# Kernel tuning notes

Hardware: AMD Instinct MI355X
Metric: run time of the kernel (lower is better)

The kernel has to match this reference:

```python
import jax, jax.numpy as jnp
import numpy as np

B, S, D, H = 2, 2048, 1024, 16
DEPTH = D // H


def setup_inputs() -> dict:
    key = jax.random.key(0)
    ks = jax.random.split(key, 10)
    batch = jax.random.normal(ks[0], (B, S, D), dtype=jnp.float32)
    # variable-length valid rows, like padded batches in the original repo
    lengths = jax.random.randint(ks[1], (B,), S // 2, S + 1)
    mask = jnp.arange(S)[None, :] < lengths[:, None]  # (B, S) bool
    scale = 1.0 / np.sqrt(D)
    Wq = jax.random.normal(ks[2], (D, D), dtype=jnp.float32) * scale
    bq = jnp.zeros((D,), dtype=jnp.float32)
    Wk = jax.random.normal(ks[3], (D, D), dtype=jnp.float32) * scale
    bk = jnp.zeros((D,), dtype=jnp.float32)
    Wv = jax.random.normal(ks[4], (D, D), dtype=jnp.float32) * scale
    bv = jnp.zeros((D,), dtype=jnp.float32)
    Wo = jax.random.normal(ks[5], (D, D), dtype=jnp.float32) * scale
    bo = jnp.zeros((D,), dtype=jnp.float32)
    return {"batch": batch, "mask": mask, "Wq": Wq, "bq": bq, "Wk": Wk,
            "bk": bk, "Wv": Wv, "bv": bv, "Wo": Wo, "bo": bo}


def _split_heads(x):
    # (B, S, D) -> (B, H, S, depth)
    b, s, _ = x.shape
    return x.reshape(b, s, H, DEPTH).transpose(0, 2, 1, 3)


def reference(batch, mask, Wq, bq, Wk, bk, Wv, bv, Wo, bo):
    b, s, _ = batch.shape
    Q = _split_heads(batch @ Wq + bq)
    K = _split_heads(batch @ Wk + bk)
    V = _split_heads(batch @ Wv + bv)
    # scaled dot-product attention with key-padding mask
    logits = jnp.einsum('bhqd,bhkd->bhqk', Q, K) / jnp.sqrt(
        jnp.asarray(DEPTH, dtype=batch.dtype))
    neg = (~mask).astype(batch.dtype) * -1e9  # (B, S)
    logits = logits + neg[:, None, None, :]
    attn = jax.nn.softmax(logits, axis=-1)
    X = jnp.einsum('bhqk,bhkd->bhqd', attn, V)
    X = X.transpose(0, 2, 1, 3).reshape(b, s, D)
    return X @ Wo + bo
```

## Files before the change

kernel.cpp:

```cpp
#include <hip/hip_runtime.h>
#include <hip/hip_bf16.h>

#define DEV __device__ __forceinline__

typedef short bf16x8 __attribute__((ext_vector_type(8)));
typedef float f32x4  __attribute__((ext_vector_type(4)));
typedef float f32x16 __attribute__((ext_vector_type(16)));

#define Bc 2
#define Sc 2048
#define Dc 1024
#define Hc 16

#define OFF_XB    0u
#define OFF_WQKVT 8388608u
#define OFF_WOT   14680064u
#define OFF_Q     16777216u
#define OFF_K     25165824u
#define OFF_VT    33554432u
#define OFF_XA    41943040u
#define OFF_BIASC 50331648u
#define OFF_LENS  50343936u

DEV short f2bf(float f) {
    __hip_bfloat16 h = __float2bfloat16(f);
    union { __hip_bfloat16 h; short s; } u; u.h = h; return u.s;
}

DEV int cvtpk(float lo, float hi_) {
    int r;
    asm("v_cvt_pk_bf16_f32 %0, %1, %2" : "=v"(r) : "v"(lo), "v"(hi_));
    return r;
}

DEV float vexp2(float x) {
    float r;
    asm("v_exp_f32 %0, %1" : "=v"(r) : "v"(x));
    return r;
}

DEV void gload16(const void* g, void* l) {
    __builtin_amdgcn_global_load_lds((const __attribute__((address_space(1))) void*)g,
                                     (__attribute__((address_space(3))) void*)l, 16, 0, 0);
}

union I4BF { int i[4]; bf16x8 v; };

DEV bf16x8 vread(const char* Vc, int row, int grp, int hi16, int rsw) {
    return *(const bf16x8*)(Vc + row * 128 + ((grp + hi16) ^ rsw));
}

__global__ __launch_bounds__(256) void prep_all_kernel(
    const float* __restrict__ batch,
    const float* __restrict__ Wq, const float* __restrict__ Wk,
    const float* __restrict__ Wv, const float* __restrict__ Wo,
    const float* __restrict__ bq, const float* __restrict__ bk, const float* __restrict__ bv,
    const unsigned char* __restrict__ mask,
    short* __restrict__ XB, short* __restrict__ WQKVT, short* __restrict__ WOT,
    float* __restrict__ biasc, int* __restrict__ lens)
{
    __shared__ float tsm[32][33];
    __shared__ int cnt;
    int blk = blockIdx.x, t = threadIdx.x;

    if (blk < 4096) {
        int i = blk * 256 + t;
        float4 v = ((const float4*)batch)[i];
        short4 o;
        o.x = f2bf(v.x); o.y = f2bf(v.y); o.z = f2bf(v.z); o.w = f2bf(v.w);
        ((short4*)XB)[i] = o;
        return;
    }
    if (blk < 8192) {
        int w = blk - 4096, z = w >> 10, tile = w & 1023;
        const float* src; short* dst;
        if (z == 0)      { src = Wq; dst = WQKVT; }
        else if (z == 1) { src = Wk; dst = WQKVT + 1024 * 1024; }
        else if (z == 2) { src = Wv; dst = WQKVT + 2 * 1024 * 1024; }
        else             { src = Wo; dst = WOT; }
        int tx = t & 31, ty = t >> 5;
        int r0 = (tile >> 5) * 32, c0 = (tile & 31) * 32;
#pragma unroll
        for (int i = 0; i < 4; i++)
            tsm[ty + i * 8][tx] = src[(size_t)(r0 + ty + i * 8) * Dc + c0 + tx];
        __syncthreads();
#pragma unroll
        for (int i = 0; i < 4; i++)
            dst[(size_t)(c0 + ty + i * 8) * Dc + r0 + tx] = f2bf(tsm[tx][ty + i * 8]);
        return;
    }
    if (blk == 8192) {
        for (int i = t; i < Dc; i += 256) {
            biasc[i] = bq[i]; biasc[Dc + i] = bk[i]; biasc[2 * Dc + i] = bv[i];
        }
        return;
    }
    {
        int b = blk - 8193;
        bool is_i32 = (mask[1] == 0);
        if (t == 0) cnt = 0;
        __syncthreads();
        int local = 0;
        for (int s = t; s < Sc; s += 256) {
            bool v = is_i32 ? (((const int*)mask)[b * Sc + s] != 0) : (mask[b * Sc + s] != 0);
            local += v ? 1 : 0;
        }
        atomicAdd(&cnt, local);
        __syncthreads();
        if (t == 0) lens[b] = cnt;
    }
}

__global__ __launch_bounds__(256) void vtrans_kernel(const short* __restrict__ V,
                                                     short* __restrict__ VT) {
    __shared__ short t[64][65];
    int tid = threadIdx.x;
    int bh = blockIdx.y, s0 = blockIdx.x * 64;
    int rr = tid >> 2, c4 = (tid & 3) * 16;
    const short* vrow = V + ((size_t)bh * Sc + s0 + rr) * 64 + c4;
    *(bf16x8*)&t[rr][c4]     = *(const bf16x8*)(vrow);
    *(bf16x8*)&t[rr][c4 + 8] = *(const bf16x8*)(vrow + 8);
    __syncthreads();
    bf16x8 a, b2;
#pragma unroll
    for (int i = 0; i < 4; i++) {
        a[i]      = t[c4 + i][rr];
        a[4 + i]  = t[c4 + 8 + i][rr];
        b2[i]     = t[c4 + 4 + i][rr];
        b2[4 + i] = t[c4 + 12 + i][rr];
    }
    short* orow = VT + ((size_t)bh * 64 + rr) * Sc + s0 + c4;
    *(bf16x8*)(orow)     = a;
    *(bf16x8*)(orow + 8) = b2;
}

__global__ __launch_bounds__(256) void gemm_qkv_kernel(
    const short* __restrict__ A, const short* __restrict__ BT, const float* __restrict__ bias,
    short* __restrict__ Qp, short* __restrict__ Kp, short* __restrict__ Vp)
{
    __shared__ short As[128 * 32];
    __shared__ short Bs[128 * 32];
    int tid = threadIdx.x, lane = tid & 63, wave = tid >> 6;
    int l15 = lane & 15, lhi = lane >> 4;
    int bm = blockIdx.x, bn = blockIdx.y;
    int wm = wave >> 1, wn = wave & 1;

    const f32x4 fzero = {0.f, 0.f, 0.f, 0.f};
    f32x4 acc[4][4];
#pragma unroll
    for (int i = 0; i < 4; i++)
#pragma unroll
        for (int j = 0; j < 4; j++) acc[i][j] = fzero;

    const char* Ab = (const char*)A;
    const char* Bb = (const char*)BT;

    for (int k0 = 0; k0 < 1024; k0 += 32) {
#pragma unroll
        for (int i = 0; i < 2; i++) {
            int o = wave * 2048 + i * 1024 + lane * 16;
            int row = o >> 6, cb = o & 63;
            gload16(Ab + ((size_t)(bm * 128 + row) * 1024 + k0) * 2 + cb,
                    (char*)As + wave * 2048 + i * 1024);
            gload16(Bb + ((size_t)(bn * 128 + row) * 1024 + k0) * 2 + cb,
                    (char*)Bs + wave * 2048 + i * 1024);
        }
        __syncthreads();
        bf16x8 af[4], bfv[4];
#pragma unroll
        for (int i = 0; i < 4; i++) {
            af[i]  = *(const bf16x8*)(As + (wm * 64 + i * 16 + l15) * 32 + lhi * 8);
            bfv[i] = *(const bf16x8*)(Bs + (wn * 64 + i * 16 + l15) * 32 + lhi * 8);
        }
#pragma unroll
        for (int i = 0; i < 4; i++)
#pragma unroll
            for (int j = 0; j < 4; j++)
                acc[i][j] = __builtin_amdgcn_mfma_f32_16x16x32_bf16(af[i], bfv[j], acc[i][j], 0, 0, 0);
        __syncthreads();
    }

#pragma unroll
    for (int i = 0; i < 4; i++)
#pragma unroll
        for (int j = 0; j < 4; j++) {
            int c = bn * 128 + wn * 64 + j * 16 + l15;
            float bc = bias[c];
            int rb = bm * 128 + wm * 64 + i * 16 + 4 * lhi;
#pragma unroll
            for (int reg = 0; reg < 4; reg++) {
                int r = rb + reg;
                float v = acc[i][j][reg] + bc;
                int which = c >> 10, cc = c & 1023, h = cc >> 6, d = cc & 63;
                int b = r >> 11, s = r & 2047;
                int bh = b * Hc + h;
                if (which == 0) v *= 0.18033688f;
                short sv = f2bf(v);
                size_t idx = ((size_t)bh * Sc + s) * 64 + d;
                if (which == 0)      Qp[idx] = sv;
                else if (which == 1) Kp[idx] = sv;
                else                 Vp[idx] = sv;
            }
        }
}

__global__ __launch_bounds__(256) void gemm_out_kernel(
    const short* __restrict__ A, const short* __restrict__ BT, const float* __restrict__ bias,
    float* __restrict__ outF)
{
    __shared__ short As[128 * 32];
    __shared__ short Bs[64 * 32];
    int tid = threadIdx.x, lane = tid & 63, wave = tid >> 6;
    int l15 = lane & 15, lhi = lane >> 4;
    int bm = blockIdx.x, bn = blockIdx.y;

    const f32x4 fzero = {0.f, 0.f, 0.f, 0.f};
    f32x4 acc[2][4];
#pragma unroll
    for (int i = 0; i < 2; i++)
#pragma unroll
        for (int j = 0; j < 4; j++) acc[i][j] = fzero;

    const char* Ab = (const char*)A;
    const char* Bb = (const char*)BT;

    for (int k0 = 0; k0 < 1024; k0 += 32) {
#pragma unroll
        for (int i = 0; i < 2; i++) {
            int o = wave * 2048 + i * 1024 + lane * 16;
            int row = o >> 6, cb = o & 63;
            gload16(Ab + ((size_t)(bm * 128 + row) * 1024 + k0) * 2 + cb,
                    (char*)As + wave * 2048 + i * 1024);
        }
        {
            int o = wave * 1024 + lane * 16;
            int row = o >> 6, cb = o & 63;
            gload16(Bb + ((size_t)(bn * 64 + row) * 1024 + k0) * 2 + cb,
                    (char*)Bs + wave * 1024);
        }
        __syncthreads();
        bf16x8 af[2], bfv[4];
#pragma unroll
        for (int i = 0; i < 2; i++)
            af[i] = *(const bf16x8*)(As + (wave * 32 + i * 16 + l15) * 32 + lhi * 8);
#pragma unroll
        for (int j = 0; j < 4; j++)
            bfv[j] = *(const bf16x8*)(Bs + (j * 16 + l15) * 32 + lhi * 8);
#pragma unroll
        for (int i = 0; i < 2; i++)
#pragma unroll
            for (int j = 0; j < 4; j++)
                acc[i][j] = __builtin_amdgcn_mfma_f32_16x16x32_bf16(af[i], bfv[j], acc[i][j], 0, 0, 0);
        __syncthreads();
    }

#pragma unroll
    for (int i = 0; i < 2; i++)
#pragma unroll
        for (int j = 0; j < 4; j++) {
            int c = bn * 64 + j * 16 + l15;
            float bc = bias[c];
            int rb = bm * 128 + wave * 32 + i * 16 + 4 * lhi;
#pragma unroll
            for (int reg = 0; reg < 4; reg++)
                outF[(size_t)(rb + reg) * Dc + c] = acc[i][j][reg] + bc;
        }
}

__global__ __launch_bounds__(128) void attn_kernel(
    const short* __restrict__ Qp, const short* __restrict__ Kp, const short* __restrict__ VTp,
    const int* __restrict__ lens, short* __restrict__ Xout)
{
    int tid = threadIdx.x, lane = tid & 63, wave = tid >> 6;
    int l31 = lane & 31, hi = lane >> 5;

    int orig = blockIdx.x;
    int xcd = orig & 7, idx = orig >> 3;
    int j = idx & 3, bx = idx >> 2;
    int bh = ((j >> 1) << 4) + xcd * 2 + (j & 1);
    int b = bh >> 4, h = bh & 15;
    int q0 = bx * 64 + wave * 32;

    __shared__ short Kt[2][64 * 64];
    __shared__ short Vt[2][64 * 64];

    const short* Qb  = Qp + (size_t)bh * Sc * 64;
    const char*  Kb  = (const char*)(Kp + (size_t)bh * Sc * 64);
    const char*  VTb = (const char*)(VTp + (size_t)bh * 64 * Sc);

    bf16x8 qf[4];
#pragma unroll
    for (int kk = 0; kk < 4; kk++)
        qf[kk] = *(const bf16x8*)(Qb + (size_t)(q0 + l31) * 64 + kk * 16 + hi * 8);

    f32x16 xacc0, xacc1, FZV;
#pragma unroll
    for (int r = 0; r < 16; r++) { xacc0[r] = 0.f; xacc1[r] = 0.f; FZV[r] = 0.f; }
    float lreg = 0.f;

    int len = lens[b];
    int nt = (len + 63) >> 6;
    int rsw = (l31 & 7) << 4;
    int hi16 = hi * 16;

#define STAGE(bufi, kt_)                                                              \
    {                                                                                 \
        int k0_ = (kt_) * 64;                                                         \
        _Pragma("unroll")                                                             \
        for (int i = 0; i < 4; i++) {                                                 \
            int o = wave * 1024 + i * 2048 + lane * 16;                               \
            int row = o >> 7, cb = o & 127;                                           \
            int scb = cb ^ ((row & 7) << 4);                                          \
            gload16(Kb + (size_t)(k0_ + row) * 128 + scb,                             \
                    (char*)&Kt[bufi][0] + wave * 1024 + i * 2048);                    \
            gload16(VTb + (size_t)row * (Sc * 2) + (size_t)k0_ * 2 + scb,             \
                    (char*)&Vt[bufi][0] + wave * 1024 + i * 2048);                    \
        }                                                                             \
    }

#define DOHALF(Kc, Vc, ROFF, KBASE, KT)                                               \
    {                                                                                 \
        __builtin_amdgcn_s_setprio(1);                                                \
        bf16x8 kf0 = *(const bf16x8*)((Kc) + (ROFF + l31) * 128 + (hi16 ^ rsw));      \
        f32x16 s = __builtin_amdgcn_mfma_f32_32x32x16_bf16(kf0, qf[0], FZV, 0, 0, 0); \
        _Pragma("unroll")                                                             \
        for (int kk = 1; kk < 4; kk++) {                                              \
            bf16x8 kf = *(const bf16x8*)((Kc) + (ROFF + l31) * 128 +                  \
                                         ((kk * 32 + hi16) ^ rsw));                   \
            s = __builtin_amdgcn_mfma_f32_32x32x16_bf16(kf, qf[kk], s, 0, 0, 0);      \
        }                                                                             \
        __builtin_amdgcn_s_setprio(0);                                                \
        if ((KT) == nt - 1) {                                                         \
            int rem = len - (KT) * 64;                                                \
            if (rem < (KBASE) + 32) {                                                 \
                _Pragma("unroll")                                                     \
                for (int r = 0; r < 16; r++) {                                        \
                    int key0 = (KBASE) + 4 * hi + (r & 3) + 8 * (r >> 2);             \
                    if (key0 >= rem) s[r] = -3.0e38f;                                 \
                }                                                                     \
            }                                                                         \
        }                                                                             \
        _Pragma("unroll")                                                             \
        for (int r = 0; r < 16; r++) s[r] = vexp2(s[r]);                              \
        {                 \
            float a0 = s[0] + s[1],   a1 = s[2] + s[3];                               \
            float a2 = s[4] + s[5],   a3 = s[6] + s[7];                               \
            float a4 = s[8] + s[9],   a5 = s[10] + s[11];                             \
            float a6 = s[12] + s[13], a7 = s[14] + s[15];                             \
            float b0 = a0 + a1, b1 = a2 + a3, b2 = a4 + a5, b3 = a6 + a7;             \
            lreg += (b0 + b1) + (b2 + b3);                                            \
        }                                                                             \
        I4BF u, w;                                                                    \
        u.i[0] = cvtpk(s[0], s[1]);   u.i[1] = cvtpk(s[2], s[3]);                     \
        u.i[2] = cvtpk(s[4], s[5]);   u.i[3] = cvtpk(s[6], s[7]);                     \
        w.i[0] = cvtpk(s[8], s[9]);   w.i[1] = cvtpk(s[10], s[11]);                   \
        w.i[2] = cvtpk(s[12], s[13]); w.i[3] = cvtpk(s[14], s[15]);                   \
        __builtin_amdgcn_s_setprio(1);                                                \
        {                                                                             \
            bf16x8 v0 = vread((Vc), l31,      (KBASE) * 2,      hi16, rsw);           \
            bf16x8 v1 = vread((Vc), 32 + l31, (KBASE) * 2,      hi16, rsw);           \
            xacc0 = __builtin_amdgcn_mfma_f32_32x32x16_bf16(v0, u.v, xacc0, 0, 0, 0); \
            xacc1 = __builtin_amdgcn_mfma_f32_32x32x16_bf16(v1, u.v, xacc1, 0, 0, 0); \
            bf16x8 v2 = vread((Vc), l31,      (KBASE) * 2 + 32, hi16, rsw);           \
            bf16x8 v3 = vread((Vc), 32 + l31, (KBASE) * 2 + 32, hi16, rsw);           \
            xacc0 = __builtin_amdgcn_mfma_f32_32x32x16_bf16(v2, w.v, xacc0, 0, 0, 0); \
            xacc1 = __builtin_amdgcn_mfma_f32_32x32x16_bf16(v3, w.v, xacc1, 0, 0, 0); \
        }                                                                             \
        __builtin_amdgcn_s_setprio(0);                                                \
    }

#define DOTILE(BUFI, KT)                                                              \
    {                                                                                 \
        const char* Kc_ = (const char*)&Kt[BUFI][0];                                  \
        const char* Vc_ = (const char*)&Vt[BUFI][0];                                  \
        DOHALF(Kc_, Vc_, 0, 0, KT);                                                   \
        DOHALF(Kc_, Vc_, 32, 32, KT);                                                 \
    }

    STAGE(0, 0);
    __syncthreads();

    int kt = 0;
    while (kt + 2 <= nt) {
        if (kt + 1 < nt) STAGE(1, kt + 1);
        DOTILE(0, kt);
        __syncthreads();
        if (kt + 2 < nt) STAGE(0, kt + 2);
        DOTILE(1, kt + 1);
        __syncthreads();
        kt += 2;
    }
    if (kt < nt) DOTILE(0, kt);

    float lfull = lreg + __shfl_xor(lreg, 32, 64);
    float rl = 1.0f / lfull;
    short* orow = Xout + (size_t)(b * Sc + q0 + l31) * Dc + h * 64;
#pragma unroll
    for (int g = 0; g < 4; g++) {
        short4 o;
        o.x = f2bf(xacc0[4 * g + 0] * rl);
        o.y = f2bf(xacc0[4 * g + 1] * rl);
        o.z = f2bf(xacc0[4 * g + 2] * rl);
        o.w = f2bf(xacc0[4 * g + 3] * rl);
        *(short4*)(orow + 4 * hi + 8 * g) = o;
    }
#pragma unroll
    for (int g = 0; g < 4; g++) {
        short4 o;
        o.x = f2bf(xacc1[4 * g + 0] * rl);
        o.y = f2bf(xacc1[4 * g + 1] * rl);
        o.z = f2bf(xacc1[4 * g + 2] * rl);
        o.w = f2bf(xacc1[4 * g + 3] * rl);
        *(short4*)(orow + 32 + 4 * hi + 8 * g) = o;
    }
}


extern "C" void kernel_launch(void* const* d_in, const int* in_sizes, int n_in,
                              void* d_out, int out_size, void* d_ws, size_t ws_size,
                              hipStream_t stream) {
    const float* batch = (const float*)d_in[0];
    const unsigned char* mask = (const unsigned char*)d_in[1];
    const float* Wq = (const float*)d_in[2];
    const float* bq = (const float*)d_in[3];
    const float* Wk = (const float*)d_in[4];
    const float* bk = (const float*)d_in[5];
    const float* Wv = (const float*)d_in[6];
    const float* bv = (const float*)d_in[7];
    const float* Wo = (const float*)d_in[8];
    const float* bo = (const float*)d_in[9];

    char* ws = (char*)d_ws;
    short* XB    = (short*)(ws + OFF_XB);
    short* WQKVT = (short*)(ws + OFF_WQKVT);
    short* WOT   = (short*)(ws + OFF_WOT);
    short* Qb    = (short*)(ws + OFF_Q);
    short* Kb    = (short*)(ws + OFF_K);
    short* VTb   = (short*)(ws + OFF_VT);
    short* XAb   = (short*)(ws + OFF_XA);
    float* BIASC = (float*)(ws + OFF_BIASC);
    int*   LENS  = (int*)(ws + OFF_LENS);
    short* Vscr  = (short*)d_out;

    prep_all_kernel<<<8195, 256, 0, stream>>>(batch, Wq, Wk, Wv, Wo, bq, bk, bv, mask,
                                              XB, WQKVT, WOT, BIASC, LENS);
    gemm_qkv_kernel<<<dim3(32, 24), 256, 0, stream>>>(XB, WQKVT, BIASC, Qb, Kb, Vscr);
    vtrans_kernel<<<dim3(32, 32), 256, 0, stream>>>(Vscr, VTb);
    attn_kernel<<<1024, 128, 0, stream>>>(Qb, Kb, VTb, LENS, XAb);
    gemm_out_kernel<<<dim3(32, 16), 256, 0, stream>>>(XAb, WOT, bo, (float*)d_out);
}
```

Baseline: 119.0 us.

## Software-pipeline attention: overlap QK/exp of tile t with PV of tile t-1

Restructures the attention main loop so each iteration computes QK logits and exponentials for the current K tile while doing the PV MFMAs for the previous tile's probabilities. Shared memory becomes one buffer holding double-buffered K and triple-buffered V, so V tiles survive an extra iteration. The intent is to hide exp/convert latency behind independent matrix work and to drop one barrier per tile pair. The cost is more registers for two sets of packed probabilities and more LDS, which may lower occupancy.

New measurement: 126.3 us. 1.06x slower.

```diff
diff --git a/kernel.cpp b/kernel.cpp
--- a/kernel.cpp
+++ b/kernel.cpp
@@ -271,6 +271,10 @@
     const short* __restrict__ Qp, const short* __restrict__ Kp, const short* __restrict__ VTp,
     const int* __restrict__ lens, short* __restrict__ Xout)
 {
+    __shared__ short KV[5 * 4096];
+    char* KtB = (char*)KV;
+    char* VtB = (char*)KV + 16384;
+
     int tid = threadIdx.x, lane = tid & 63, wave = tid >> 6;
     int l31 = lane & 31, hi = lane >> 5;
 
@@ -281,9 +285,6 @@
     int b = bh >> 4, h = bh & 15;
     int q0 = bx * 64 + wave * 32;
 
-    __shared__ short Kt[2][64 * 64];
-    __shared__ short Vt[2][64 * 64];
-
     const short* Qb  = Qp + (size_t)bh * Sc * 64;
     const char*  Kb  = (const char*)(Kp + (size_t)bh * Sc * 64);
     const char*  VTb = (const char*)(VTp + (size_t)bh * 64 * Sc);
@@ -303,7 +304,7 @@
     int rsw = (l31 & 7) << 4;
     int hi16 = hi * 16;
 
-#define STAGE(bufi, kt_)                                                              \
+#define STAGE(koff, voff, kt_)                                                        \
     {                                                                                 \
         int k0_ = (kt_) * 64;                                                         \
         _Pragma("unroll")                                                             \
@@ -312,20 +313,21 @@
             int row = o >> 7, cb = o & 127;                                           \
             int scb = cb ^ ((row & 7) << 4);                                          \
             gload16(Kb + (size_t)(k0_ + row) * 128 + scb,                             \
-                    (char*)&Kt[bufi][0] + wave * 1024 + i * 2048);                    \
+                    KtB + (koff) + wave * 1024 + i * 2048);                           \
             gload16(VTb + (size_t)row * (Sc * 2) + (size_t)k0_ * 2 + scb,             \
-                    (char*)&Vt[bufi][0] + wave * 1024 + i * 2048);                    \
+                    VtB + (voff) + wave * 1024 + i * 2048);                           \
         }                                                                             \
     }
 
-#define DOHALF(Kc, Vc, ROFF, KBASE, KT)                                               \
+#define QKHALF(U, W, ROFF, KBASE, koff, KT)                                           \
     {                                                                                 \
+        const char* Kc = KtB + (koff);                                                \
         __builtin_amdgcn_s_setprio(1);                                                \
-        bf16x8 kf0 = *(const bf16x8*)((Kc) + (ROFF + l31) * 128 + (hi16 ^ rsw));      \
+        bf16x8 kf0 = *(const bf16x8*)(Kc + (ROFF + l31) * 128 + (hi16 ^ rsw));        \
         f32x16 s = __builtin_amdgcn_mfma_f32_32x32x16_bf16(kf0, qf[0], FZV, 0, 0, 0); \
         _Pragma("unroll")                                                             \
         for (int kk = 1; kk < 4; kk++) {                                              \
-            bf16x8 kf = *(const bf16x8*)((Kc) + (ROFF + l31) * 128 +                  \
+            bf16x8 kf = *(const bf16x8*)(Kc + (ROFF + l31) * 128 +                    \
                                          ((kk * 32 + hi16) ^ rsw));                   \
             s = __builtin_amdgcn_mfma_f32_32x32x16_bf16(kf, qf[kk], s, 0, 0, 0);      \
         }                                                                             \
@@ -342,7 +344,7 @@
         }                                                                             \
         _Pragma("unroll")                                                             \
         for (int r = 0; r < 16; r++) s[r] = vexp2(s[r]);                              \
-        {                 \
+        {                                                                             \
             float a0 = s[0] + s[1],   a1 = s[2] + s[3];                               \
             float a2 = s[4] + s[5],   a3 = s[6] + s[7];                               \
             float a4 = s[8] + s[9],   a5 = s[10] + s[11];                             \
@@ -350,47 +352,66 @@
             float b0 = a0 + a1, b1 = a2 + a3, b2 = a4 + a5, b3 = a6 + a7;             \
             lreg += (b0 + b1) + (b2 + b3);                                            \
         }                                                                             \
-        I4BF u, w;                                                                    \
-        u.i[0] = cvtpk(s[0], s[1]);   u.i[1] = cvtpk(s[2], s[3]);                     \
-        u.i[2] = cvtpk(s[4], s[5]);   u.i[3] = cvtpk(s[6], s[7]);                     \
-        w.i[0] = cvtpk(s[8], s[9]);   w.i[1] = cvtpk(s[10], s[11]);                   \
-        w.i[2] = cvtpk(s[12], s[13]); w.i[3] = cvtpk(s[14], s[15]);                   \
+        U.i[0] = cvtpk(s[0], s[1]);   U.i[1] = cvtpk(s[2], s[3]);                     \
+        U.i[2] = cvtpk(s[4], s[5]);   U.i[3] = cvtpk(s[6], s[7]);                     \
+        W.i[0] = cvtpk(s[8], s[9]);   W.i[1] = cvtpk(s[10], s[11]);                   \
+        W.i[2] = cvtpk(s[12], s[13]); W.i[3] = cvtpk(s[14], s[15]);                   \
+    }
+
+#define QKEXP(U0, W0, U1, W1, koff, KT)                                               \
+    {                                                                                 \
+        QKHALF(U0, W0, 0, 0, koff, KT);                                               \
+        QKHALF(U1, W1, 32, 32, koff, KT);                                             \
+    }
+
+#define PVSTEP(U0, W0, U1, W1, voff)                                                  \
+    {                                                                                 \
+        const char* Vc = VtB + (voff);                                                \
         __builtin_amdgcn_s_setprio(1);                                                \
-        {                                                                             \
-            bf16x8 v0 = vread((Vc), l31,      (KBASE) * 2,      hi16, rsw);           \
-            bf16x8 v1 = vread((Vc), 32 + l31, (KBASE) * 2,      hi16, rsw);           \
-            xacc0 = __builtin_amdgcn_mfma_f32_32x32x16_bf16(v0, u.v, xacc0, 0, 0, 0); \
-            xacc1 = __builtin_amdgcn_mfma_f32_32x32x16_bf16(v1, u.v, xacc1, 0, 0, 0); \
-            bf16x8 v2 = vread((Vc), l31,      (KBASE) * 2 + 32, hi16, rsw);           \
-            bf16x8 v3 = vread((Vc), 32 + l31, (KBASE) * 2 + 32, hi16, rsw);           \
-            xacc0 = __builtin_amdgcn_mfma_f32_32x32x16_bf16(v2, w.v, xacc0, 0, 0, 0); \
-            xacc1 = __builtin_amdgcn_mfma_f32_32x32x16_bf16(v3, w.v, xacc1, 0, 0, 0); \
-        }                                                                             \
+        bf16x8 v0 = vread(Vc, l31,      0,  hi16, rsw);                               \
+        bf16x8 v1 = vread(Vc, 32 + l31, 0,  hi16, rsw);                               \
+        xacc0 = __builtin_amdgcn_mfma_f32_32x32x16_bf16(v0, U0.v, xacc0, 0, 0, 0);    \
+        xacc1 = __builtin_amdgcn_mfma_f32_32x32x16_bf16(v1, U0.v, xacc1, 0, 0, 0);    \
+        bf16x8 v2 = vread(Vc, l31,      32, hi16, rsw);                               \
+        bf16x8 v3 = vread(Vc, 32 + l31, 32, hi16, rsw);                               \
+        xacc0 = __builtin_amdgcn_mfma_f32_32x32x16_bf16(v2, W0.v, xacc0, 0, 0, 0);    \
+        xacc1 = __builtin_amdgcn_mfma_f32_32x32x16_bf16(v3, W0.v, xacc1, 0, 0, 0);    \
+        bf16x8 v4 = vread(Vc, l31,      64, hi16, rsw);                               \
+        bf16x8 v5 = vread(Vc, 32 + l31, 64, hi16, rsw);                               \
+        xacc0 = __builtin_amdgcn_mfma_f32_32x32x16_bf16(v4, U1.v, xacc0, 0, 0, 0);    \
+        xacc1 = __builtin_amdgcn_mfma_f32_32x32x16_bf16(v5, U1.v, xacc1, 0, 0, 0);    \
+        bf16x8 v6 = vread(Vc, l31,      96, hi16, rsw);                               \
+        bf16x8 v7 = vread(Vc, 32 + l31, 96, hi16, rsw);                               \
+        xacc0 = __builtin_amdgcn_mfma_f32_32x32x16_bf16(v6, W1.v, xacc0, 0, 0, 0);    \
+        xacc1 = __builtin_amdgcn_mfma_f32_32x32x16_bf16(v7, W1.v, xacc1, 0, 0, 0);    \
         __builtin_amdgcn_s_setprio(0);                                                \
     }
 
-#define DOTILE(BUFI, KT)                                                              \
-    {                                                                                 \
-        const char* Kc_ = (const char*)&Kt[BUFI][0];                                  \
-        const char* Vc_ = (const char*)&Vt[BUFI][0];                                  \
-        DOHALF(Kc_, Vc_, 0, 0, KT);                                                   \
-        DOHALF(Kc_, Vc_, 32, 32, KT);                                                 \
-    }
-
-    STAGE(0, 0);
+    I4BF uA0, wA0, uA1, wA1, uB0, wB0, uB1, wB1;
+
+    STAGE(0, 0, 0);
     __syncthreads();
-
-    int kt = 0;
-    while (kt + 2 <= nt) {
-        if (kt + 1 < nt) STAGE(1, kt + 1);
-        DOTILE(0, kt);
-        __syncthreads();
-        if (kt + 2 < nt) STAGE(0, kt + 2);
-        DOTILE(1, kt + 1);
-        __syncthreads();
-        kt += 2;
-    }
-    if (kt < nt) DOTILE(0, kt);
+    if (nt > 1) STAGE(8192, 8192, 1);
+    QKEXP(uA0, wA0, uA1, wA1, 0, 0);
+    __syncthreads();
+
+    int vprev = 0, vcur = 1, vnext = 2;
+    for (int t = 1; t < nt; ++t) {
+        int kc = (t & 1) << 13;
+        int kn = ((t + 1) & 1) << 13;
+        if (t + 1 < nt) STAGE(kn, vnext << 13, t + 1);
+        if (t & 1) {
+            QKEXP(uB0, wB0, uB1, wB1, kc, t);
+            PVSTEP(uA0, wA0, uA1, wA1, vprev << 13);
+        } else {
+            QKEXP(uA0, wA0, uA1, wA1, kc, t);
+            PVSTEP(uB0, wB0, uB1, wB1, vprev << 13);
+        }
+        __syncthreads();
+        vprev = vcur; vcur = vnext; vnext = (vnext == 2) ? 0 : vnext + 1;
+    }
+    if ((nt - 1) & 1) { PVSTEP(uB0, wB0, uB1, wB1, vprev << 13); }
+    else              { PVSTEP(uA0, wA0, uA1, wA1, vprev << 13); }
 
     float lfull = lreg + __shfl_xor(lreg, 32, 64);
     float rl = 1.0f / lfull;
```
